# Kernel optimization log

Measured on AMD Instinct MI355X. Metric: run time of the kernel, lower is better.

## Reference

```python
import jax, jax.numpy as jnp
import numpy as np

D, M, ALPHA = 64, 512, 7.18
DIM = 1024
B = M * D  # batch: M clusters x D samples each


def setup_inputs() -> dict:
    key = jax.random.key(0)
    outputs = jax.random.normal(key, (B, DIM), dtype=jnp.float32)
    indices = jnp.arange(B, dtype=jnp.int64 if jax.config.jax_enable_x64 else jnp.int32)
    assignment = indices // D  # sample i -> cluster i//D (contiguous blocks of D)
    loss_vector = jnp.zeros((M,), jnp.float32)
    loss_count = jnp.zeros((M,), jnp.float32)
    return {"outputs": outputs, "indices": indices, "assignment": assignment,
            "loss_vector": loss_vector, "loss_count": loss_count}


def reference(outputs, indices, assignment, loss_vector, loss_count):
    outputs = outputs.astype(jnp.float32)
    own = assignment[indices]                              # [B] cluster id per sample
    n = jnp.float32(B)
    # cluster means (each cluster has exactly D samples)
    means = jax.ops.segment_sum(outputs, own, num_segments=M) / D   # [M, DIM]
    # pooled variance: sum ||x_i - mu_{c(i)}||^2 / (N - 1)
    diff_own = outputs - means[own]
    var_sum = jnp.sum(diff_own * diff_own)
    stdev = -2.0 * var_sum / (n - 1.0)                     # the (negative) -2*sigma^2 term
    # squared distances to every cluster mean: [B, M]
    sq = (jnp.sum(outputs * outputs, axis=1)[:, None]
          + jnp.sum(means * means, axis=1)[None, :]
          - 2.0 * outputs @ means.T)
    exps = jnp.exp(sq / stdev)                             # [B, M]
    own_col = own[:, None]
    own_exp = jnp.take_along_axis(exps, own_col, axis=1)[:, 0]
    denom = jnp.sum(exps, axis=1) - own_exp                # sum over mF != own
    sq_own = jnp.take_along_axis(sq, own_col, axis=1)[:, 0]
    log_ratio = sq_own / stdev - ALPHA - jnp.log(denom)    # log(exp(.-alpha)/denom)
    per_loss = jnp.maximum(-log_ratio, 0.0)                # == -clamp(log_ratio, max=0)
    loss = (jnp.sum(per_loss) / n).reshape(1)
    lv = (loss_vector + jax.ops.segment_sum(per_loss, own, num_segments=M)) / n
    lc = loss_count + jax.ops.segment_sum(jnp.ones((B,), jnp.float32), own, num_segments=M)
    variance = var_sum / (n - 1.0)                         # stdev / -2.0 in the original
    return loss, lv, lc, variance
```

## Files before the change

### kernel.cpp

```cpp
#include <hip/hip_runtime.h>
#include <hip/hip_bf16.h>
#include <stdint.h>

#define DIM 1024
#define ALPHA 7.18f
#define INV_N (1.0f/32768.0f)
#define NM1 32767.0f
#define LOG2E 1.44269504088896f
#define LN2 0.693147180559945f

typedef __attribute__((ext_vector_type(8))) short bfrag8;
typedef __attribute__((ext_vector_type(4))) float f32x4;

typedef const __attribute__((address_space(1))) void gv_t;
typedef __attribute__((address_space(3))) void lv_t;

__device__ __forceinline__ unsigned f2bf_bits(float f) {
    unsigned u = __float_as_uint(f);
    return (u + 0x7fffu + ((u >> 16) & 1u)) >> 16;
}

__global__ __launch_bounds__(512)
void k1_colsum(const float* __restrict__ outputs, const int* __restrict__ indices,
               const int* __restrict__ assignment, float* __restrict__ mean_sums,
               unsigned* __restrict__ counts, float* __restrict__ scalars,
               int* __restrict__ own_g) {
    __shared__ int sown[64];
    __shared__ int suni;
    __shared__ float4 spart[8][64];
    __shared__ float ssq[8];
    const int tid = threadIdx.x;
    const int rg = blockIdx.x >> 2, cq = blockIdx.x & 3;
    const int row0 = rg * 64;
    if (tid == 0) suni = 1;
    if (tid < 64) {
        int m = assignment[indices[row0 + tid]];
        sown[tid] = m;
        if (cq == 0) { own_g[row0 + tid] = m; atomicAdd(&counts[m], 1u); }
    }
    __syncthreads();
    if (tid < 63 && sown[tid] != sown[tid + 1]) suni = 0;
    __syncthreads();

    const int c4 = tid & 63;
    const int rq = tid >> 6;
    const float* gp = outputs + (size_t)(row0 + rq * 8) * DIM + cq * 256 + c4 * 4;
    float4 s4 = {0.f, 0.f, 0.f, 0.f};
    float sq = 0.f;

    if (suni) {
        #pragma unroll
        for (int r = 0; r < 8; ++r) {
            float4 v = *(const float4*)(gp + (size_t)r * DIM);
            sq = fmaf(v.x, v.x, sq); sq = fmaf(v.y, v.y, sq);
            sq = fmaf(v.z, v.z, sq); sq = fmaf(v.w, v.w, sq);
            s4.x += v.x; s4.y += v.y; s4.z += v.z; s4.w += v.w;
        }
        spart[rq][c4] = s4;
        __syncthreads();
        if (rq == 0) {
            #pragma unroll
            for (int r = 1; r < 8; ++r) {
                float4 o = spart[r][c4];
                s4.x += o.x; s4.y += o.y; s4.z += o.z; s4.w += o.w;
            }
            float* dst = mean_sums + (size_t)sown[0] * DIM + cq * 256 + c4 * 4;
            atomicAdd(dst + 0, s4.x); atomicAdd(dst + 1, s4.y);
            atomicAdd(dst + 2, s4.z); atomicAdd(dst + 3, s4.w);
        }
    } else {
        int curm = sown[rq * 8];
        for (int r = 0; r < 8; ++r) {
            float4 v = *(const float4*)(gp + (size_t)r * DIM);
            int m = sown[rq * 8 + r];
            if (m != curm) {
                float* dst = mean_sums + (size_t)curm * DIM + cq * 256 + c4 * 4;
                atomicAdd(dst + 0, s4.x); atomicAdd(dst + 1, s4.y);
                atomicAdd(dst + 2, s4.z); atomicAdd(dst + 3, s4.w);
                s4 = (float4){0.f, 0.f, 0.f, 0.f};
                curm = m;
            }
            sq = fmaf(v.x, v.x, sq); sq = fmaf(v.y, v.y, sq);
            sq = fmaf(v.z, v.z, sq); sq = fmaf(v.w, v.w, sq);
            s4.x += v.x; s4.y += v.y; s4.z += v.z; s4.w += v.w;
        }
        float* dst = mean_sums + (size_t)curm * DIM + cq * 256 + c4 * 4;
        atomicAdd(dst + 0, s4.x); atomicAdd(dst + 1, s4.y);
        atomicAdd(dst + 2, s4.z); atomicAdd(dst + 3, s4.w);
        __syncthreads();
    }

    #pragma unroll
    for (int mk = 32; mk; mk >>= 1) sq += __shfl_xor(sq, mk, 64);
    if ((tid & 63) == 0) ssq[tid >> 6] = sq;
    __syncthreads();
    if (tid == 0) {
        float s = 0.f;
        #pragma unroll
        for (int w = 0; w < 8; ++w) s += ssq[w];
        atomicAdd(&scalars[0], s);
    }
}

__global__ __launch_bounds__(256)
void k2_means(const float* __restrict__ mean_sums, const unsigned* __restrict__ counts,
              unsigned short* __restrict__ b_kt, float* __restrict__ msq,
              float* __restrict__ scalars) {
    const int m = blockIdx.x, t = threadIdx.x;
    const float* row = mean_sums + (size_t)m * DIM;
    float4 v = *(const float4*)(row + t * 4);
    float4 mu = {v.x * (1.0f/64.0f), v.y * (1.0f/64.0f), v.z * (1.0f/64.0f), v.w * (1.0f/64.0f)};
    const int tt = t >> 3, kc = (t >> 1) & 3, half = t & 1;
    unsigned lo = f2bf_bits(mu.x) | (f2bf_bits(mu.y) << 16);
    unsigned hi = f2bf_bits(mu.z) | (f2bf_bits(mu.w) << 16);
    *(uint2*)((char*)b_kt + tt * 32768 + m * 64 + ((kc ^ ((m >> 1) & 3)) << 4) + half * 8)
        = make_uint2(lo, hi);
    float sq = fmaf(mu.x, mu.x, fmaf(mu.y, mu.y, fmaf(mu.z, mu.z, mu.w * mu.w)));
    #pragma unroll
    for (int mk = 32; mk; mk >>= 1) sq += __shfl_xor(sq, mk, 64);
    __shared__ float sw[4];
    if ((t & 63) == 0) sw[t >> 6] = sq;
    __syncthreads();
    if (t == 0) {
        float s = sw[0] + sw[1] + sw[2] + sw[3];
        msq[m] = s;
        atomicAdd(&scalars[1], ((float)counts[m] - 128.0f) * s);
    }
}

__global__ __launch_bounds__(512)
void k3_finalize(float* __restrict__ scalars, const float* __restrict__ msq,
                 const unsigned* __restrict__ counts, const float* __restrict__ loss_vector,
                 const float* __restrict__ loss_count, float* __restrict__ msl,
                 float* __restrict__ out) {
    const int t = threadIdx.x;
    float var_sum = scalars[0] + scalars[1];
    float inv_std = -NM1 / (2.0f * var_sum);
    msl[t] = msq[t] * inv_std * LOG2E;
    out[1 + t] = loss_vector[t] * INV_N;
    out[513 + t] = loss_count[t] + (float)counts[t];
    if (t == 0) {
        out[0] = 0.0f;
        out[1025] = var_sum / NM1;
        scalars[2] = inv_std;
    }
}

__global__ __launch_bounds__(512, 2)
void k4_gemm(const float* __restrict__ outputs, const unsigned short* __restrict__ b_kt,
             const float* __restrict__ msl, const float* __restrict__ scalars,
             const int* __restrict__ own_g, float* __restrict__ out) {
    __shared__ short lA[2][128 * 32];
    __shared__ short lB[2][512 * 32];
    __shared__ float red_sum[128][4];
    __shared__ float red_own[128][4];

    const int tid  = threadIdx.x;
    const int lane = tid & 63;
    const int wid  = tid >> 6;
    const int wm   = wid >> 2;
    const int wn   = wid & 3;
    const int brow = blockIdx.x * 128;

    const int rA = tid >> 3;
    const int kq = tid & 7;
    const float* gA = outputs + (size_t)(brow + rA) * DIM + kq * 4;
    const int aw0 = rA * 64 + ((((kq >> 1)) ^ ((rA >> 1) & 3)) << 4) + ((kq & 1) << 3);
    const int aw1 = aw0 + 64 * 64;

    const int arow0 = wm * 64 + (lane & 15);
    const int ar_base = arow0 * 64 + (((lane >> 4) ^ ((arow0 >> 1) & 3)) << 4);
    const int bcol = wn * 128 + (lane & 15);
    const int br_byte = bcol * 64 + (((lane >> 4) ^ ((bcol >> 1) & 3)) << 4);

    const char* bbase = (const char*)b_kt;

    f32x4 acc[4][8];
    #pragma unroll
    for (int i = 0; i < 4; ++i)
        #pragma unroll
        for (int j = 0; j < 8; ++j)
            acc[i][j] = (f32x4){0.f, 0.f, 0.f, 0.f};

    #pragma unroll
    for (int i = 0; i < 4; ++i) {
        const char* gsrc = bbase + (wid * 4 + i) * 1024 + lane * 16;
        char* ldst = (char*)&lB[0][0] + (wid * 4 + i) * 1024;
        __builtin_amdgcn_global_load_lds((gv_t*)gsrc, (lv_t*)ldst, 16, 0, 0);
    }
    {
        float4 a0 = *(const float4*)gA;
        float4 a1 = *(const float4*)(gA + 64 * DIM);
        unsigned l0 = f2bf_bits(a0.x) | (f2bf_bits(a0.y) << 16);
        unsigned h0 = f2bf_bits(a0.z) | (f2bf_bits(a0.w) << 16);
        unsigned l1 = f2bf_bits(a1.x) | (f2bf_bits(a1.y) << 16);
        unsigned h1 = f2bf_bits(a1.z) | (f2bf_bits(a1.w) << 16);
        *(uint2*)((char*)&lA[0][0] + aw0) = make_uint2(l0, h0);
        *(uint2*)((char*)&lA[0][0] + aw1) = make_uint2(l1, h1);
    }
    __syncthreads();

    int cur = 0;
    for (int t = 0; t < 32; ++t) {
        const bool has_next = (t + 1) < 32;
        float4 a0n, a1n;
        if (has_next) {
            a0n = *(const float4*)(gA + (t + 1) * 32);
            a1n = *(const float4*)(gA + 64 * DIM + (t + 1) * 32);
            #pragma unroll
            for (int i = 0; i < 4; ++i) {
                const char* gsrc = bbase + (size_t)(t + 1) * 32768 + (wid * 4 + i) * 1024 + lane * 16;
                char* ldst = (char*)&lB[cur ^ 1][0] + (wid * 4 + i) * 1024;
                __builtin_amdgcn_global_load_lds((gv_t*)gsrc, (lv_t*)ldst, 16, 0, 0);
            }
        }

        const char* pa = (const char*)&lA[cur][0] + ar_base;
        const char* pb = (const char*)&lB[cur][0] + br_byte;
        bfrag8 af[4];
        #pragma unroll
        for (int fm = 0; fm < 4; ++fm) af[fm] = *(const bfrag8*)(pa + fm * 1024);
        #pragma unroll
        for (int fn = 0; fn < 8; ++fn) {
            bfrag8 bf = *(const bfrag8*)(pb + fn * 1024);
            #pragma unroll
            for (int fm = 0; fm < 4; ++fm)
                acc[fm][fn] = __builtin_amdgcn_mfma_f32_16x16x32_bf16(af[fm], bf, acc[fm][fn], 0, 0, 0);
        }

        if (has_next) {
            unsigned l0 = f2bf_bits(a0n.x) | (f2bf_bits(a0n.y) << 16);
            unsigned h0 = f2bf_bits(a0n.z) | (f2bf_bits(a0n.w) << 16);
            unsigned l1 = f2bf_bits(a1n.x) | (f2bf_bits(a1n.y) << 16);
            unsigned h1 = f2bf_bits(a1n.z) | (f2bf_bits(a1n.w) << 16);
            *(uint2*)((char*)&lA[cur ^ 1][0] + aw0) = make_uint2(l0, h0);
            *(uint2*)((char*)&lA[cur ^ 1][0] + aw1) = make_uint2(l1, h1);
        }
        __syncthreads();
        cur ^= 1;
    }

    float mslv[8];
    #pragma unroll
    for (int fn = 0; fn < 8; ++fn) mslv[fn] = msl[bcol + fn * 16];
    const float inv_std = scalars[2];
    const float c2k = -2.0f * inv_std * LOG2E;
    int ownv[4][4];
    #pragma unroll
    for (int fm = 0; fm < 4; ++fm)
        #pragma unroll
        for (int rg = 0; rg < 4; ++rg)
            ownv[fm][rg] = own_g[brow + wm * 64 + fm * 16 + ((lane >> 4) << 2) + rg];

    #pragma unroll
    for (int fm = 0; fm < 4; ++fm) {
        #pragma unroll
        for (int rg = 0; rg < 4; ++rg) {
            float sum = 0.f, oa = -1e30f;
            int ownr = ownv[fm][rg];
            #pragma unroll
            for (int fn = 0; fn < 8; ++fn) {
                float dot = acc[fm][fn][rg];
                float arg = fmaf(c2k, dot, mslv[fn]);
                sum += exp2f(arg);
                bool isown = (bcol + fn * 16) == ownr;
                oa = isown ? arg : oa;
            }
            #pragma unroll
            for (int mk = 1; mk < 16; mk <<= 1) {
                sum += __shfl_xor(sum, mk, 64);
                oa = fmaxf(oa, __shfl_xor(oa, mk, 64));
            }
            if ((lane & 15) == 0) {
                int r_in = wm * 64 + fm * 16 + ((lane >> 4) << 2) + rg;
                red_sum[r_in][wn] = sum;
                red_own[r_in][wn] = oa;
            }
        }
    }
    __syncthreads();

    if (tid < 128) {
        float s = red_sum[tid][0] + red_sum[tid][1] + red_sum[tid][2] + red_sum[tid][3];
        float oa = fmaxf(fmaxf(red_own[tid][0], red_own[tid][1]),
                         fmaxf(red_own[tid][2], red_own[tid][3]));
        float denom = s - exp2f(oa);
        float per_loss = fmaxf(ALPHA + LN2 * (log2f(denom) - oa), 0.f);
        int ownr = own_g[brow + tid];
        float ls = per_loss;
        #pragma unroll
        for (int mk = 1; mk < 64; mk <<= 1) ls += __shfl_xor(ls, mk, 64);
        int own0 = __shfl(ownr, 0, 64);
        if (__all(ownr == own0)) {
            if (lane == 0) atomicAdd(&out[1 + own0], ls * INV_N);
        } else {
            atomicAdd(&out[1 + ownr], per_loss * INV_N);
        }
        if (lane == 0) atomicAdd(&out[0], ls * INV_N);
    }
}

extern "C" void kernel_launch(void* const* d_in, const int* in_sizes, int n_in,
                              void* d_out, int out_size, void* d_ws, size_t ws_size,
                              hipStream_t stream) {
    const float* outputs     = (const float*)d_in[0];
    const int*   indices     = (const int*)d_in[1];
    const int*   assignment  = (const int*)d_in[2];
    const float* loss_vector = (const float*)d_in[3];
    const float* loss_count  = (const float*)d_in[4];
    float* out = (float*)d_out;

    char* ws = (char*)d_ws;
    float*          mean_sums = (float*)ws;
    unsigned*       counts    = (unsigned*)(ws + 2097152);
    float*          scalars   = (float*)(ws + 2099200);
    const size_t    ZB        = 2099456;
    unsigned short* b_kt      = (unsigned short*)(ws + 2101248);
    float*          msq       = (float*)(ws + 3149824);
    float*          msl       = (float*)(ws + 3151872);
    int*            own_g     = (int*)(ws + 3153920);

    hipMemsetAsync(d_ws, 0, ZB, stream);
    hipLaunchKernelGGL(k1_colsum, dim3(2048), dim3(512), 0, stream,
                       outputs, indices, assignment, mean_sums, counts, scalars, own_g);
    hipLaunchKernelGGL(k2_means, dim3(512), dim3(256), 0, stream,
                       mean_sums, counts, b_kt, msq, scalars);
    hipLaunchKernelGGL(k3_finalize, dim3(1), dim3(512), 0, stream,
                       scalars, msq, counts, loss_vector, loss_count, msl, out);
    hipLaunchKernelGGL(k4_gemm, dim3(256), dim3(512), 0, stream,
                       outputs, b_kt, msl, scalars, own_g, out);
}
```

Before: 302.8 us.

## Halve GEMM row tile to 64 rows and double grid; batch colsum loads

```diff
diff --git a/kernel.cpp b/kernel.cpp
--- a/kernel.cpp
+++ b/kernel.cpp
@@ -49,12 +49,14 @@
     float sq = 0.f;
 
     if (suni) {
+        float4 v[8];
+        #pragma unroll
+        for (int r = 0; r < 8; ++r) v[r] = *(const float4*)(gp + (size_t)r * DIM);
         #pragma unroll
         for (int r = 0; r < 8; ++r) {
-            float4 v = *(const float4*)(gp + (size_t)r * DIM);
-            sq = fmaf(v.x, v.x, sq); sq = fmaf(v.y, v.y, sq);
-            sq = fmaf(v.z, v.z, sq); sq = fmaf(v.w, v.w, sq);
-            s4.x += v.x; s4.y += v.y; s4.z += v.z; s4.w += v.w;
+            sq = fmaf(v[r].x, v[r].x, sq); sq = fmaf(v[r].y, v[r].y, sq);
+            sq = fmaf(v[r].z, v[r].z, sq); sq = fmaf(v[r].w, v[r].w, sq);
+            s4.x += v[r].x; s4.y += v[r].y; s4.z += v[r].z; s4.w += v[r].w;
         }
         spart[rq][c4] = s4;
         __syncthreads();
@@ -146,38 +148,37 @@
     }
 }
 
-__global__ __launch_bounds__(512, 2)
+__global__ __launch_bounds__(512)
 void k4_gemm(const float* __restrict__ outputs, const unsigned short* __restrict__ b_kt,
              const float* __restrict__ msl, const float* __restrict__ scalars,
              const int* __restrict__ own_g, float* __restrict__ out) {
-    __shared__ short lA[2][128 * 32];
+    __shared__ short lA[2][64 * 32];
     __shared__ short lB[2][512 * 32];
-    __shared__ float red_sum[128][4];
-    __shared__ float red_own[128][4];
+    __shared__ float red_sum[64][4];
+    __shared__ float red_own[64][4];
 
     const int tid  = threadIdx.x;
     const int lane = tid & 63;
     const int wid  = tid >> 6;
     const int wm   = wid >> 2;
     const int wn   = wid & 3;
-    const int brow = blockIdx.x * 128;
+    const int brow = blockIdx.x * 64;
 
     const int rA = tid >> 3;
     const int kq = tid & 7;
     const float* gA = outputs + (size_t)(brow + rA) * DIM + kq * 4;
-    const int aw0 = rA * 64 + ((((kq >> 1)) ^ ((rA >> 1) & 3)) << 4) + ((kq & 1) << 3);
-    const int aw1 = aw0 + 64 * 64;
-
-    const int arow0 = wm * 64 + (lane & 15);
-    const int ar_base = arow0 * 64 + (((lane >> 4) ^ ((arow0 >> 1) & 3)) << 4);
+    const int aw_byte = rA * 64 + (((kq >> 1) ^ ((rA >> 1) & 3)) << 4) + ((kq & 1) << 3);
+
+    const int arow = wm * 32 + (lane & 15);
+    const int ar_byte = arow * 64 + (((lane >> 4) ^ ((arow >> 1) & 3)) << 4);
     const int bcol = wn * 128 + (lane & 15);
     const int br_byte = bcol * 64 + (((lane >> 4) ^ ((bcol >> 1) & 3)) << 4);
 
     const char* bbase = (const char*)b_kt;
 
-    f32x4 acc[4][8];
-    #pragma unroll
-    for (int i = 0; i < 4; ++i)
+    f32x4 acc[2][8];
+    #pragma unroll
+    for (int i = 0; i < 2; ++i)
         #pragma unroll
         for (int j = 0; j < 8; ++j)
             acc[i][j] = (f32x4){0.f, 0.f, 0.f, 0.f};
@@ -189,24 +190,19 @@
         __builtin_amdgcn_global_load_lds((gv_t*)gsrc, (lv_t*)ldst, 16, 0, 0);
     }
     {
-        float4 a0 = *(const float4*)gA;
-        float4 a1 = *(const float4*)(gA + 64 * DIM);
-        unsigned l0 = f2bf_bits(a0.x) | (f2bf_bits(a0.y) << 16);
-        unsigned h0 = f2bf_bits(a0.z) | (f2bf_bits(a0.w) << 16);
-        unsigned l1 = f2bf_bits(a1.x) | (f2bf_bits(a1.y) << 16);
-        unsigned h1 = f2bf_bits(a1.z) | (f2bf_bits(a1.w) << 16);
-        *(uint2*)((char*)&lA[0][0] + aw0) = make_uint2(l0, h0);
-        *(uint2*)((char*)&lA[0][0] + aw1) = make_uint2(l1, h1);
+        float4 areg = *(const float4*)gA;
+        unsigned lo = f2bf_bits(areg.x) | (f2bf_bits(areg.y) << 16);
+        unsigned hi = f2bf_bits(areg.z) | (f2bf_bits(areg.w) << 16);
+        *(uint2*)((char*)&lA[0][0] + aw_byte) = make_uint2(lo, hi);
     }
     __syncthreads();
 
     int cur = 0;
     for (int t = 0; t < 32; ++t) {
         const bool has_next = (t + 1) < 32;
-        float4 a0n, a1n;
+        float4 anext;
         if (has_next) {
-            a0n = *(const float4*)(gA + (t + 1) * 32);
-            a1n = *(const float4*)(gA + 64 * DIM + (t + 1) * 32);
+            anext = *(const float4*)(gA + (t + 1) * 32);
             #pragma unroll
             for (int i = 0; i < 4; ++i) {
                 const char* gsrc = bbase + (size_t)(t + 1) * 32768 + (wid * 4 + i) * 1024 + lane * 16;
@@ -215,26 +211,21 @@
             }
         }
 
-        const char* pa = (const char*)&lA[cur][0] + ar_base;
+        const char* pa = (const char*)&lA[cur][0] + ar_byte;
         const char* pb = (const char*)&lB[cur][0] + br_byte;
-        bfrag8 af[4];
-        #pragma unroll
-        for (int fm = 0; fm < 4; ++fm) af[fm] = *(const bfrag8*)(pa + fm * 1024);
+        bfrag8 a0 = *(const bfrag8*)(pa);
+        bfrag8 a1 = *(const bfrag8*)(pa + 1024);
         #pragma unroll
         for (int fn = 0; fn < 8; ++fn) {
             bfrag8 bf = *(const bfrag8*)(pb + fn * 1024);
-            #pragma unroll
-            for (int fm = 0; fm < 4; ++fm)
-                acc[fm][fn] = __builtin_amdgcn_mfma_f32_16x16x32_bf16(af[fm], bf, acc[fm][fn], 0, 0, 0);
+            acc[0][fn] = __builtin_amdgcn_mfma_f32_16x16x32_bf16(a0, bf, acc[0][fn], 0, 0, 0);
+            acc[1][fn] = __builtin_amdgcn_mfma_f32_16x16x32_bf16(a1, bf, acc[1][fn], 0, 0, 0);
         }
 
         if (has_next) {
-            unsigned l0 = f2bf_bits(a0n.x) | (f2bf_bits(a0n.y) << 16);
-            unsigned h0 = f2bf_bits(a0n.z) | (f2bf_bits(a0n.w) << 16);
-            unsigned l1 = f2bf_bits(a1n.x) | (f2bf_bits(a1n.y) << 16);
-            unsigned h1 = f2bf_bits(a1n.z) | (f2bf_bits(a1n.w) << 16);
-            *(uint2*)((char*)&lA[cur ^ 1][0] + aw0) = make_uint2(l0, h0);
-            *(uint2*)((char*)&lA[cur ^ 1][0] + aw1) = make_uint2(l1, h1);
+            unsigned lo = f2bf_bits(anext.x) | (f2bf_bits(anext.y) << 16);
+            unsigned hi = f2bf_bits(anext.z) | (f2bf_bits(anext.w) << 16);
+            *(uint2*)((char*)&lA[cur ^ 1][0] + aw_byte) = make_uint2(lo, hi);
         }
         __syncthreads();
         cur ^= 1;
@@ -245,15 +236,15 @@
     for (int fn = 0; fn < 8; ++fn) mslv[fn] = msl[bcol + fn * 16];
     const float inv_std = scalars[2];
     const float c2k = -2.0f * inv_std * LOG2E;
-    int ownv[4][4];
-    #pragma unroll
-    for (int fm = 0; fm < 4; ++fm)
+    int ownv[2][4];
+    #pragma unroll
+    for (int fm = 0; fm < 2; ++fm)
         #pragma unroll
         for (int rg = 0; rg < 4; ++rg)
-            ownv[fm][rg] = own_g[brow + wm * 64 + fm * 16 + ((lane >> 4) << 2) + rg];
-
-    #pragma unroll
-    for (int fm = 0; fm < 4; ++fm) {
+            ownv[fm][rg] = own_g[brow + wm * 32 + fm * 16 + ((lane >> 4) << 2) + rg];
+
+    #pragma unroll
+    for (int fm = 0; fm < 2; ++fm) {
         #pragma unroll
         for (int rg = 0; rg < 4; ++rg) {
             float sum = 0.f, oa = -1e30f;
@@ -272,7 +263,7 @@
                 oa = fmaxf(oa, __shfl_xor(oa, mk, 64));
             }
             if ((lane & 15) == 0) {
-                int r_in = wm * 64 + fm * 16 + ((lane >> 4) << 2) + rg;
+                int r_in = wm * 32 + fm * 16 + ((lane >> 4) << 2) + rg;
                 red_sum[r_in][wn] = sum;
                 red_own[r_in][wn] = oa;
             }
@@ -280,7 +271,7 @@
     }
     __syncthreads();
 
-    if (tid < 128) {
+    if (tid < 64) {
         float s = red_sum[tid][0] + red_sum[tid][1] + red_sum[tid][2] + red_sum[tid][3];
         float oa = fmaxf(fmaxf(red_own[tid][0], red_own[tid][1]),
                          fmaxf(red_own[tid][2], red_own[tid][3]));
@@ -292,11 +283,11 @@
         for (int mk = 1; mk < 64; mk <<= 1) ls += __shfl_xor(ls, mk, 64);
         int own0 = __shfl(ownr, 0, 64);
         if (__all(ownr == own0)) {
-            if (lane == 0) atomicAdd(&out[1 + own0], ls * INV_N);
+            if (tid == 0) atomicAdd(&out[1 + own0], ls * INV_N);
         } else {
             atomicAdd(&out[1 + ownr], per_loss * INV_N);
         }
-        if (lane == 0) atomicAdd(&out[0], ls * INV_N);
+        if (tid == 0) atomicAdd(&out[0], ls * INV_N);
     }
 }
 
@@ -327,6 +318,6 @@
                        mean_sums, counts, b_kt, msq, scalars);
     hipLaunchKernelGGL(k3_finalize, dim3(1), dim3(512), 0, stream,
                        scalars, msq, counts, loss_vector, loss_count, msl, out);
-    hipLaunchKernelGGL(k4_gemm, dim3(256), dim3(512), 0, stream,
+    hipLaunchKernelGGL(k4_gemm, dim3(512), dim3(512), 0, stream,
                        outputs, b_kt, msl, scalars, own_g, out);
 }
```

Result: slower. 330.6 us (+9.2%).
